# Kernel optimization log

Hardware: AMD Instinct MI355X
Metric: run time of the kernel (lower is better)

Reference implementation:

```python
import jax, jax.numpy as jnp
import numpy as np

N_NODES = 100000
N_USER = 50000
D_IN = 100     # n_units[0]
F_OUT = 16     # n_units[1]
N_HEAD = 3     # n_heads[0]
N_TYPES = 3    # nb_nodes
N_EDGES = 1600000
D2 = 128


def setup_inputs() -> dict:
    key = jax.random.key(0)
    ks = jax.random.split(key, 9)
    h = jax.random.normal(ks[0], (N_NODES, D_IN), dtype=jnp.float32)
    edge_index = jax.random.randint(ks[1], (N_TYPES, 2, N_EDGES), 0, N_NODES, dtype=jnp.int64)
    # per-type GAT params (torch Linear stored transposed: (in, out))
    W = jax.random.normal(ks[2], (N_TYPES, D_IN, N_HEAD * F_OUT), dtype=jnp.float32) * 0.1
    b = jax.random.normal(ks[3], (N_TYPES, N_HEAD * F_OUT), dtype=jnp.float32) * 0.1
    a_src = jax.random.normal(ks[4], (N_TYPES, N_HEAD, F_OUT), dtype=jnp.float32) * 0.1
    a_trg = jax.random.normal(ks[5], (N_TYPES, N_HEAD, F_OUT), dtype=jnp.float32) * 0.1
    # additive attention params
    w1 = jax.random.normal(ks[6], (D_IN, D2), dtype=jnp.float32) * 0.1
    w2 = jax.random.normal(ks[7], (F_OUT, D2), dtype=jnp.float32) * 0.1
    m = jax.random.normal(ks[8], (D2, 1), dtype=jnp.float32) * 0.1
    return {"h": h, "W": W, "b": b, "a_src": a_src, "a_trg": a_trg,
            "w1": w1, "w2": w2, "m": m, "edge_index": edge_index}


def _sparse_gat(h, src, trg, W, b, a_src, a_trg):
    """Single SparseMultiHeadGraphAttention layer followed by head-mean."""
    N = h.shape[0]
    h_prime = (h @ W + b).reshape(N, N_HEAD, F_OUT)  # (N, H, F)
    hs = h_prime[src]                                # (E', H, F) edge gather
    # NOTE: faithful to source — both scores use the src-gathered features
    e = (hs * a_src).sum(-1) + (hs * a_trg).sum(-1)  # (E', H)
    e = jax.nn.leaky_relu(e, negative_slope=0.2)
    e = e - e.max()                                  # global max (as in source)
    exp_e = jnp.exp(e)
    denom = jax.ops.segment_sum(exp_e, trg, num_segments=N)      # (N, H)
    alpha = exp_e / (denom[trg] + 1e-10)                          # (E', H)
    out = jax.ops.segment_sum(hs * alpha[..., None], trg, num_segments=N)  # (N, H, F)
    return out.mean(axis=1)  # == permute(1,0,2).mean(dim=0)


def reference(h, W, b, a_src, a_trg, w1, w2, m, edge_index):
    N = h.shape[0]
    loop = jnp.arange(N, dtype=edge_index.dtype)
    embs = []
    for t in range(N_TYPES):  # small fixed set of relation types
        src = jnp.concatenate([edge_index[t, 0], loop])  # add self-loops
        trg = jnp.concatenate([edge_index[t, 1], loop])
        x = _sparse_gat(h, src, trg, W[t], b[t], a_src[t], a_trg[t])
        embs.append(x[:N_USER])
    type_aware = jnp.stack(embs, axis=1)  # (Nu, |Rs|, F)
    feat = h[:N_USER]                     # (Nu, D)
    # additive attention over types
    q = jnp.tanh((feat @ w1)[:, None, :] + type_aware @ w2)  # (Nu, |Rs|, D2)
    scores = (q @ m)[..., 0]                                  # (Nu, |Rs|)
    beta = jax.nn.softmax(scores, axis=1)
    fusion = jnp.einsum('nr,nrf->nf', beta, type_aware)[:, None, :]  # (Nu,1,F)
    return jnp.concatenate([fusion, type_aware], axis=1)  # (Nu, |Rs|+1, F)
```

## Files before the change

kernel.cpp:

```cpp
#include <hip/hip_runtime.h>
#include <hip/hip_bf16.h>

#define N_NODES 100000
#define N_USER  50000
#define D_IN    100
#define F_OUT   16
#define N_HEAD  3
#define N_TYPES 3
#define N_EDGES 1600000
#define D2      128
#define N_SEG   (N_TYPES * N_USER)
#define KP      136
#define CAP     64
#define CAPH    32
#define NBLK    ((N_NODES + 63) / 64)
#define NPAIR   (N_TYPES * N_EDGES / 2)
#define NBIN    256
#define SEGB    586
#define NBLKA   782
#define PAIRS_A 3072
#define CAPPB   40
#define NPREPB  270
#define NPLACE  512

typedef __hip_bfloat16 bf16;
typedef __attribute__((ext_vector_type(8))) short bf16x8;
typedef __attribute__((ext_vector_type(4))) float f32x4;
static __device__ __forceinline__ float b2f(bf16 x) { return __bfloat162float(x); }
static __device__ __forceinline__ float us2f(ushort u) { return __uint_as_float(((unsigned)u) << 16); }

#define OFF_CVT   64
#define OFF_CW    (OFF_CVT)
#define OFF_CB    (OFF_CW + 14400)
#define OFF_CAS   (OFF_CB + 144)
#define OFF_CAT   (OFF_CAS + 144)
#define OFF_CW1   (OFF_CAT + 144)
#define OFF_CW2   (OFF_CW1 + 12800)
#define OFF_CM    (OFF_CW2 + 2048)
#define CVT_TOTAL 29808
#define OFF_WT    29888
#define OFF_REC   49472
#define OFF_BUCKET (OFF_REC + 9600000 + 240000 + 302000 + 9600000 + 2400000 + 6406144)
#define OFF_CPB   (OFF_REC + 9600000)
#define OFF_CA    (OFF_CPB + 240000)
#define OFF_CB2   (OFF_CA + 151000)
#define OFF_ELIST (OFF_CB2 + 151000)
#define OFF_TA    (OFF_ELIST + 9600000)
#define OFF_FW1   (OFF_TA + 2400000)

static __device__ __forceinline__ int2 load_ei2(const void* ei, int f64, size_t pairPos) {
    if (f64) {
        int4 v = ((const int4*)ei)[pairPos];
        int2 r; r.x = v.x; r.y = v.z; return r;
    }
    return ((const int2*)ei)[pairPos];
}

#define NBLK_CVT 117
__global__ __launch_bounds__(256) void k_prep_part(
        const void* __restrict__ W, const void* __restrict__ b,
        const void* __restrict__ as_, const void* __restrict__ at_,
        const void* __restrict__ w1, const void* __restrict__ w2,
        const void* __restrict__ m, const void* __restrict__ ei,
        const unsigned* __restrict__ hraw,
        float* __restrict__ cvt, ushort* __restrict__ wt,
        unsigned* __restrict__ bucket, unsigned* __restrict__ cpb) {
    __shared__ int bc[NBIN];
    __shared__ int s_sane, s_nz;
    const int tid = threadIdx.x;
    if (tid == 0) { s_sane = 0; s_nz = 0; }
    if (tid < NBIN) bc[tid] = 0;
    __syncthreads();
    {
        const unsigned* eir = (const unsigned*)ei;
        int cnt = 0; unsigned o = 0;
        for (int i = tid; i < 1024; i += 256) {
            unsigned w = hraw[i];
            unsigned e = (w >> 23) & 0xFF;
            if (e >= 64 && e <= 200) cnt++;
            o |= eir[2 * i + 1];
        }
        atomicAdd(&s_sane, cnt);
        atomicOr(&s_nz, (int)(o != 0));
    }
    __syncthreads();
    const int f32in = (s_sane > 512);
    const int f64ei = s_nz ? 0 : 1;
    if (blockIdx.x < NBLK_CVT) {
        int i = blockIdx.x * 256 + tid;
        if (i < CVT_TOTAL) {
            const void* src; int off;
            if      (i < 14400)                 { src = W;   off = i; }
            else if (i < 14400+144)             { src = b;   off = i - 14400; }
            else if (i < 14400+288)             { src = as_; off = i - 14544; }
            else if (i < 14400+432)             { src = at_; off = i - 14688; }
            else if (i < 14400+432+12800)       { src = w1;  off = i - 14832; }
            else if (i < 14400+432+12800+2048)  { src = w2;  off = i - 27632; }
            else                                { src = m;   off = i - 29680; }
            cvt[i] = f32in ? ((const float*)src)[off] : b2f(((const bf16*)src)[off]);
        }
    } else if (blockIdx.x < NPREPB) {
        int i = (blockIdx.x - NBLK_CVT) * 256 + tid;
        if (i < 6 * 48 * KP) {
            int g = i / (48 * KP);
            int r = i - g * (48 * KP);
            int n = r / KP, k = r % KP;
            ushort v = 0;
            if (k < D_IN) {
                if (g < 3) {
                    size_t src = ((size_t)g * D_IN + k) * 48 + n;
                    if (f32in) { bf16 x = __float2bfloat16(((const float*)W)[src]); v = *(ushort*)&x; }
                    else       { v = ((const ushort*)W)[src]; }
                } else {
                    int c = (g - 3) * 48 + n;
                    if (c < D2) {
                        size_t src = (size_t)k * D2 + c;
                        if (f32in) { bf16 x = __float2bfloat16(((const float*)w1)[src]); v = *(ushort*)&x; }
                        else       { v = ((const ushort*)w1)[src]; }
                    }
                }
            }
            wt[i] = v;
        }
    } else {
        const int blk = blockIdx.x - NPREPB;
        const int NE2 = N_EDGES >> 1;
        const int pair0 = blk * PAIRS_A;
        int npair = NPAIR - pair0; if (npair > PAIRS_A) npair = PAIRS_A;
#pragma unroll
        for (int q = 0; q < PAIRS_A / 256; ++q) {
            int pp = q * 256 + tid;
            int ok = (pp < npair);
            int pg = pair0 + (ok ? pp : 0);
            int t  = (pg >= 2 * NE2) ? 2 : ((pg >= NE2) ? 1 : 0);
            int ep = pg - t * NE2;
            int2 tg = load_ei2(ei, f64ei, (size_t)(t * 2 + 1) * NE2 + ep);
            int2 sr = load_ei2(ei, f64ei, (size_t)(t * 2) * NE2 + ep);
            if (ok && (unsigned)tg.x < N_USER) {
                int seg = t * N_USER + tg.x;
                int bin = seg & 255;
                int pos = atomicAdd(&bc[bin], 1);
                if (pos < CAPPB)
                    bucket[((size_t)bin * NBLKA + blk) * CAPPB + pos] =
                        ((unsigned)(seg >> 8) << 17) | (unsigned)sr.x;
            }
            if (ok && (unsigned)tg.y < N_USER) {
                int seg = t * N_USER + tg.y;
                int bin = seg & 255;
                int pos = atomicAdd(&bc[bin], 1);
                if (pos < CAPPB)
                    bucket[((size_t)bin * NBLKA + blk) * CAPPB + pos] =
                        ((unsigned)(seg >> 8) << 17) | (unsigned)sr.y;
            }
        }
        __syncthreads();
        if (tid < NBIN) cpb[(size_t)tid * NBLKA + blk] = (unsigned)bc[tid];
    }
}

__global__ __launch_bounds__(256) void k_place_pack(
        const unsigned* __restrict__ bucket, const unsigned* __restrict__ cpb,
        int* __restrict__ elist, unsigned* __restrict__ cA,
        unsigned* __restrict__ cBv,
        const void* __restrict__ h, const ushort* __restrict__ wtg,
        const float* __restrict__ cb, const float* __restrict__ cas,
        const float* __restrict__ cat,
        ushort* __restrict__ fw1G, float* __restrict__ rec) {
    __shared__ alignas(16) unsigned char smem[17408];
    __shared__ int s_sane;
    const int tid = threadIdx.x;
    if (blockIdx.x < NPLACE) {
        int* sc = (int*)smem;
        const int bin = blockIdx.x >> 1;
        const int hf  = blockIdx.x & 1;
        for (int i = tid; i < SEGB; i += 256) sc[i] = 0;
        __syncthreads();
        const int rn = NBLKA / 2;
        for (int j = tid; j < rn; j += 256) {
            int r = 2 * j + hf;
            int c = (int)cpb[(size_t)bin * NBLKA + r];
            if (c > CAPPB) c = CAPPB;
            size_t base = ((size_t)bin * NBLKA + r) * CAPPB;
            for (int i4 = 0; i4 < (c + 3) >> 2; ++i4) {
                uint4 wv = *(const uint4*)&bucket[base + 4 * i4];
#pragma unroll
                for (int k = 0; k < 4; ++k) {
                    int idx = 4 * i4 + k;
                    if (idx < c) {
                        unsigned e = (k == 0) ? wv.x : (k == 1) ? wv.y : (k == 2) ? wv.z : wv.w;
                        int sl  = (int)(e >> 17);
                        int src = (int)(e & 0x1FFFFu);
                        int pos = atomicAdd(&sc[sl], 1);
                        if (pos < CAPH) {
                            int seg = (sl << 8) + bin;
                            int t = seg / N_USER;
                            elist[(size_t)seg * CAP + (hf << 5) + pos] =
                                (t * N_NODES + src) << 7;
                        }
                    }
                }
            }
        }
        __syncthreads();
        for (int s = tid; s < SEGB; s += 256) {
            int seg = (s << 8) + bin;
            if (seg < N_SEG) {
                int cc = sc[s]; if (cc > CAPH) cc = CAPH;
                if (hf) cBv[seg] = (unsigned)cc; else cA[seg] = (unsigned)cc;
            }
        }
    } else {
        if (tid == 0) s_sane = 0;
        __syncthreads();
        {
            const unsigned* hraw = (const unsigned*)h;
            int cnt = 0;
            for (int i = tid; i < 1024; i += 256) {
                unsigned e = (hraw[i] >> 23) & 0xFF;
                if (e >= 64 && e <= 200) cnt++;
            }
            atomicAdd(&s_sane, cnt);
        }
        __syncthreads();
        const int f32in = (s_sane > 512);
        ushort (*hs)[KP] = reinterpret_cast<ushort(*)[KP]>(smem);
        const int node0 = (blockIdx.x - NPLACE) * 64;
        if (f32in) {
            const float* hfp = (const float*)h;
            for (int i = tid; i < 64 * 25; i += 256) {
                int r = i / 25, ch = i - r * 25;
                int n = node0 + r;
                ushort4 s4 = make_ushort4(0, 0, 0, 0);
                if (n < N_NODES) {
                    float4 x = *(const float4*)&hfp[(size_t)n * D_IN + ch * 4];
                    bf16 b0 = __float2bfloat16(x.x), b1 = __float2bfloat16(x.y);
                    bf16 b2 = __float2bfloat16(x.z), b3 = __float2bfloat16(x.w);
                    s4 = make_ushort4(*(ushort*)&b0, *(ushort*)&b1, *(ushort*)&b2, *(ushort*)&b3);
                }
                *(ushort4*)&hs[r][ch * 4] = s4;
            }
        } else {
            const ushort* hu = (const ushort*)h;
            for (int i = tid; i < 64 * 25; i += 256) {
                int r = i / 25, ch = i - r * 25;
                int n = node0 + r;
                uint2 v = make_uint2(0, 0);
                if (n < N_NODES)
                    v = *(const uint2*)&hu[(size_t)n * D_IN + ch * 4];
                *(uint2*)&hs[r][ch * 4] = v;
            }
        }
        for (int i = tid; i < 64 * 9; i += 256) {
            int r = i / 9, ch = i - r * 9;
            *(uint2*)&hs[r][100 + ch * 4] = make_uint2(0, 0);
        }
        __syncthreads();
        const int lane = tid & 63;
        const int w    = tid >> 6;
        const int m    = lane & 15;
        const int quad = lane >> 4;
        const int elig = (node0 < N_USER);
        const int nphase = elig ? 6 : 3;
        char* recc = (char*)rec;
        for (int p = 0; p < nphase; ++p) {
            const ushort* wp = wtg + (size_t)p * 48 * KP;
            f32x4 acc0 = {0.f, 0.f, 0.f, 0.f}, acc1 = acc0, acc2 = acc0;
#pragma unroll
            for (int ks = 0; ks < 4; ++ks) {
                int ko = ks * 32 + quad * 8;
                bf16x8 a  = *(const bf16x8*)&hs[w * 16 + m][ko];
                bf16x8 b0 = *(const bf16x8*)&wp[(0 * 16 + m) * KP + ko];
                bf16x8 b1 = *(const bf16x8*)&wp[(1 * 16 + m) * KP + ko];
                bf16x8 b2 = *(const bf16x8*)&wp[(2 * 16 + m) * KP + ko];
                acc0 = __builtin_amdgcn_mfma_f32_16x16x32_bf16(a, b0, acc0, 0, 0, 0);
                acc1 = __builtin_amdgcn_mfma_f32_16x16x32_bf16(a, b1, acc1, 0, 0, 0);
                acc2 = __builtin_amdgcn_mfma_f32_16x16x32_bf16(a, b2, acc2, 0, 0, 0);
            }
            if (p < 3) {
                const int t = p;
                float hpv[3][4], sred[3][4];
#pragma unroll
                for (int nt = 0; nt < 3; ++nt) {
                    int col = nt * 16 + m;
                    float bv = cb[t * 48 + col];
                    float av = cas[t * 48 + col] + cat[t * 48 + col];
                    f32x4 a4 = (nt == 0) ? acc0 : (nt == 1) ? acc1 : acc2;
#pragma unroll
                    for (int r = 0; r < 4; ++r) {
                        hpv[nt][r] = a4[r] + bv;
                        sred[nt][r] = hpv[nt][r] * av;
                    }
                }
#pragma unroll
                for (int d = 1; d < 16; d <<= 1) {
#pragma unroll
                    for (int nt = 0; nt < 3; ++nt)
#pragma unroll
                        for (int r = 0; r < 4; ++r)
                            sred[nt][r] += __shfl_xor(sred[nt][r], d);
                }
                float pk[3][4];
#pragma unroll
                for (int nt = 0; nt < 3; ++nt)
#pragma unroll
                    for (int r = 0; r < 4; ++r) {
                        float s = sred[nt][r];
                        s = (s > 0.f) ? s : 0.2f * s;
                        pk[nt][r] = __expf(s);
                    }
#pragma unroll
                for (int nt = 0; nt < 3; ++nt) {
                    int colb = (nt * 16 + m) * 2;
#pragma unroll
                    for (int r = 0; r < 4; ++r) {
                        int n = node0 + w * 16 + quad * 4 + r;
                        if (n < N_NODES) {
                            bf16 gb = __float2bfloat16(pk[nt][r] * hpv[nt][r]);
                            *(ushort*)(recc + (((size_t)t * N_NODES + n) << 7) + colb) = *(ushort*)&gb;
                        }
                    }
                }
                if (m < 3) {
#pragma unroll
                    for (int r = 0; r < 4; ++r) {
                        int n = node0 + w * 16 + quad * 4 + r;
                        if (n < N_NODES)
                            *(float*)(recc + (((size_t)t * N_NODES + n) << 7) + 96 + m * 4) = pk[m][r];
                    }
                }
            } else {
                const int chunk = p - 3;
#pragma unroll
                for (int nt = 0; nt < 3; ++nt) {
                    int col = chunk * 48 + nt * 16 + m;
                    if (col < D2) {
                        f32x4 a4 = (nt == 0) ? acc0 : (nt == 1) ? acc1 : acc2;
#pragma unroll
                        for (int r = 0; r < 4; ++r) {
                            int row = w * 16 + quad * 4 + r;
                            int v = node0 + row;
                            if (v < N_USER) {
                                bf16 fb = __float2bfloat16(a4[r]);
                                fw1G[(size_t)v * D2 + col] = *(ushort*)&fb;
                            }
                        }
                    }
                }
            }
        }
    }
}

__global__ __launch_bounds__(256) void k_gather(const float* __restrict__ rec,
                                                const int* __restrict__ elist,
                                                const unsigned* __restrict__ cA,
                                                const unsigned* __restrict__ cBv,
                                                float* __restrict__ ta) {
    int wid = (blockIdx.x * 256 + threadIdx.x) >> 6;
    if (wid >= N_SEG) return;
    int lane = threadIdx.x & 63;
    int t = wid / N_USER, v = wid - t * N_USER;
    int h = lane >> 5, l = lane & 31;
    const char* recc = (const char*)rec;
    const unsigned l4 = (unsigned)(l << 2);
    const bool isg = (l < 24);
    const int      s0m = isg ? 16 : 0;
    const unsigned m0  = isg ? 0xFFFF0000u : 0xFFFFFFFFu;
    const unsigned m1  = isg ? 0xFFFF0000u : 0u;
    int ev = elist[(size_t)wid * CAP + lane];
    int a = (int)cA[wid];
    int b = (int)cBv[wid];
    unsigned wself = 0u;
    if (h == 0)
        wself = *(const unsigned*)(recc + (((unsigned)(t * N_NODES + v)) << 7) + l4);
    float a0 = 0.f, a1 = 0.f;
    const int myn = h ? b : a;
    const int mx = a > b ? a : b;
    const int hbase = h << 5;
    for (int i0 = 0; i0 < mx; i0 += 12) {
        unsigned w[12];
#pragma unroll
        for (int q = 0; q < 12; ++q) {
            w[q] = 0u;
            int ee = i0 + q;
            int off = __shfl(ev, hbase + (ee & 31));
            if (ee < myn)
                w[q] = *(const unsigned*)(recc + (unsigned)off + l4);
        }
        __builtin_amdgcn_sched_barrier(0);
#pragma unroll
        for (int q = 0; q < 12; ++q) {
            a0 += __uint_as_float((w[q] << s0m) & m0);
            a1 += __uint_as_float(w[q] & m1);
        }
    }
    a0 += __uint_as_float((wself << s0m) & m0);
    a1 += __uint_as_float(wself & m1);
    a0 += __shfl_xor(a0, 32);
    a1 += __shfl_xor(a1, 32);
    int k = (l >> 3); if (k > 2) k = 2;
    float dk = __shfl(a0, 24 + k) + 1e-10f;
    float r0 = a0 / dk, r1 = a1 / dk;
    float sf0 = r0 + __shfl(r0, (l & 7) + 8) + __shfl(r0, (l & 7) + 16);
    float sf1 = r1 + __shfl(r1, (l & 7) + 8) + __shfl(r1, (l & 7) + 16);
    if (lane < 8) {
        float2 o;
        o.x = sf0 * (1.f / 3.f);
        o.y = sf1 * (1.f / 3.f);
        *(float2*)&ta[(size_t)v * 48 + t * 16 + 2 * lane] = o;
    }
}

__global__ __launch_bounds__(256) void k_fuse(const ushort* __restrict__ fw1G,
                                              const float* __restrict__ cw2,
                                              const float* __restrict__ cm,
                                              const float* __restrict__ ta,
                                              const unsigned* __restrict__ hraw,
                                              void* __restrict__ out) {
    __shared__ float w2s[F_OUT * D2];
    __shared__ float ms[D2];
    __shared__ float tas[64][49];
    __shared__ float psum[64][12];
    __shared__ float fus[64][16];
    __shared__ int s_sane;
    const int tid = threadIdx.x;
    const int v0 = blockIdx.x * 64;
    if (tid == 0) s_sane = 0;
    __syncthreads();
    {
        int cnt = 0;
        for (int i = tid; i < 1024; i += 256) {
            unsigned e = (hraw[i] >> 23) & 0xFF;
            if (e >= 64 && e <= 200) cnt++;
        }
        atomicAdd(&s_sane, cnt);
    }
    for (int i = tid; i < F_OUT * D2; i += 256) w2s[i] = cw2[i];
    if (tid < D2) ms[tid] = cm[tid];
    {
        int r = tid >> 2, c4 = (tid & 3) * 12;
        int v = v0 + r;
        for (int j = 0; j < 12; ++j)
            tas[r][c4 + j] = (v < N_USER) ? ta[(size_t)v * 48 + c4 + j] : 0.f;
    }
    __syncthreads();
    const int f32in = (s_sane > 512);
    const int u  = tid & 63;
    const int og = tid >> 6;
    const int v  = v0 + u;
    float tr[48];
#pragma unroll
    for (int x = 0; x < 48; ++x) tr[x] = tas[u][x];
    float acc[2][16];
#pragma unroll
    for (int ph = 0; ph < 2; ++ph) {
        if (v < N_USER) {
            const ushort* fr = fw1G + (size_t)v * D2 + ph * 64 + og * 16;
            ushort us[16];
            *(uint4*)&us[0] = *(const uint4*)&fr[0];
            *(uint4*)&us[8] = *(const uint4*)&fr[8];
#pragma unroll
            for (int j = 0; j < 16; ++j) acc[ph][j] = us2f(us[j]);
        } else {
#pragma unroll
            for (int j = 0; j < 16; ++j) acc[ph][j] = 0.f;
        }
    }
    float part[3] = {0.f, 0.f, 0.f};
#pragma unroll
    for (int ph = 0; ph < 2; ++ph) {
#pragma unroll
        for (int j = 0; j < 16; ++j) {
            int c = ph * 64 + og * 16 + j;
            float fv = acc[ph][j];
            float mv = ms[c];
#pragma unroll
            for (int t = 0; t < 3; ++t) {
                float z = fv;
#pragma unroll
                for (int f = 0; f < 16; ++f)
                    z += tr[t * 16 + f] * w2s[f * D2 + c];
                float q = 1.f - 2.f / (__expf(2.f * z) + 1.f);
                part[t] += q * mv;
            }
        }
    }
    psum[u][og * 3 + 0] = part[0];
    psum[u][og * 3 + 1] = part[1];
    psum[u][og * 3 + 2] = part[2];
    __syncthreads();
    if (tid < 64) {
        float sc[3];
#pragma unroll
        for (int t = 0; t < 3; ++t)
            sc[t] = psum[tid][t] + psum[tid][3 + t] + psum[tid][6 + t] + psum[tid][9 + t];
        float mx = fmaxf(sc[0], fmaxf(sc[1], sc[2]));
        float e0 = __expf(sc[0] - mx), e1 = __expf(sc[1] - mx), e2 = __expf(sc[2] - mx);
        float inv = 1.f / (e0 + e1 + e2);
#pragma unroll
        for (int f = 0; f < 16; ++f)
            fus[tid][f] = (e0 * tas[tid][f] + e1 * tas[tid][16 + f] + e2 * tas[tid][32 + f]) * inv;
    }
    __syncthreads();
    for (int kq = 0; kq < 16; ++kq) {
        int lin = kq * 256 + tid;
        int r = lin >> 6, c = lin & 63;
        int vv = v0 + r;
        if (vv < N_USER) {
            float val = (c < 16) ? fus[r][c] : tas[r][c - 16];
            size_t oidx = (size_t)vv * 64 + c;
            if (f32in) ((float*)out)[oidx] = val;
            else       ((bf16*)out)[oidx]  = __float2bfloat16(val);
        }
    }
}

extern "C" void kernel_launch(void* const* d_in, const int* in_sizes, int n_in,
                              void* d_out, int out_size, void* d_ws, size_t ws_size,
                              hipStream_t stream) {
    float* ws = (float*)d_ws;
    float* cvt   = ws + OFF_CVT;
    float* cb    = ws + OFF_CB;
    float* cas   = ws + OFF_CAS;
    float* cat   = ws + OFF_CAT;
    float* cw2   = ws + OFF_CW2;
    float* cm    = ws + OFF_CM;
    ushort* wt   = (ushort*)(ws + OFF_WT);
    float* rec   = ws + OFF_REC;
    unsigned* bucket = (unsigned*)(ws + OFF_BUCKET);
    unsigned* cpb    = (unsigned*)(ws + OFF_CPB);
    unsigned* cA     = (unsigned*)(ws + OFF_CA);
    unsigned* cBv    = (unsigned*)(ws + OFF_CB2);
    int*   elist = (int*)(ws + OFF_ELIST);
    float* ta    = ws + OFF_TA;
    ushort* fw1  = (ushort*)(ws + OFF_FW1);

    k_prep_part<<<NPREPB + NBLKA, 256, 0, stream>>>(
        d_in[1], d_in[2], d_in[3], d_in[4], d_in[5], d_in[6], d_in[7], d_in[8],
        (const unsigned*)d_in[0], cvt, wt, bucket, cpb);

    k_place_pack<<<NPLACE + NBLK, 256, 0, stream>>>(
        bucket, cpb, elist, cA, cBv,
        d_in[0], wt, cb, cas, cat, fw1, rec);

    k_gather<<<(N_SEG * 64 + 255) / 256, 256, 0, stream>>>(rec, elist, cA, cBv, ta);

    k_fuse<<<(N_USER + 63) / 64, 256, 0, stream>>>(
        fw1, cw2, cm, ta, (const unsigned*)d_in[0], d_out);
}
```

Before: 358.4 us.

## Fuse four pipeline kernels into one cooperative persistent kernel with grid syncs

Merges the prep/partition, place/pack, gather and fuse kernels into a single cooperative kernel that grid-strides over each stage's blocks and separates stages with grid-wide syncs. This removes three kernel launches and the idle gaps between them. The grid is sized from the occupancy query, capped at 8 blocks per CU times 256 CUs, and falls back to the old multi-kernel path if the cooperative launch fails. The risk is that grid syncs and persistent looping cut parallelism or occupancy in the gather-heavy stages, since every block also reserves about 21 KB of shared memory.

After: 375.8 us. 1.05x slower.

```diff
diff --git a/kernel.cpp b/kernel.cpp
--- a/kernel.cpp
+++ b/kernel.cpp
@@ -1,5 +1,8 @@
 #include <hip/hip_runtime.h>
 #include <hip/hip_bf16.h>
+#include <hip/hip_cooperative_groups.h>
+
+namespace cg = cooperative_groups;
 
 #define N_NODES 100000
 #define N_USER  50000
@@ -22,6 +25,8 @@
 #define CAPPB   40
 #define NPREPB  270
 #define NPLACE  512
+#define NFUSE   ((N_USER + 63) / 64)
+#define NBLK_CVT 117
 
 typedef __hip_bfloat16 bf16;
 typedef __attribute__((ext_vector_type(8))) short bf16x8;
@@ -30,8 +35,7 @@
 static __device__ __forceinline__ float us2f(ushort u) { return __uint_as_float(((unsigned)u) << 16); }
 
 #define OFF_CVT   64
-#define OFF_CW    (OFF_CVT)
-#define OFF_CB    (OFF_CW + 14400)
+#define OFF_CB    (OFF_CVT + 14400)
 #define OFF_CAS   (OFF_CB + 144)
 #define OFF_CAT   (OFF_CAS + 144)
 #define OFF_CW1   (OFF_CAT + 144)
@@ -56,7 +60,435 @@
     return ((const int2*)ei)[pairPos];
 }
 
-#define NBLK_CVT 117
+struct MegaArgs {
+    const void *h, *W, *b, *as_, *at_, *w1, *w2, *m, *ei;
+    float* cvt; ushort* wt;
+    unsigned *bucket, *cpb, *cA, *cBv;
+    int* elist;
+    float* ta; ushort* fw1; float* rec;
+    const float *cb, *cas, *cat, *cw2, *cm;
+    void* out;
+};
+
+__global__ __launch_bounds__(256) void kmega(MegaArgs A) {
+    __shared__ alignas(16) unsigned char arena[21248];
+    __shared__ int s_flags[2];
+    const int tid = threadIdx.x;
+    const int bid = blockIdx.x;
+    const int gs  = gridDim.x;
+    cg::grid_group gg = cg::this_grid();
+    if (tid == 0) { s_flags[0] = 0; s_flags[1] = 0; }
+    __syncthreads();
+    {
+        const unsigned* hraw = (const unsigned*)A.h;
+        const unsigned* eir  = (const unsigned*)A.ei;
+        int cnt = 0; unsigned o = 0;
+        for (int i = tid; i < 1024; i += 256) {
+            unsigned e = (hraw[i] >> 23) & 0xFF;
+            cnt += (e >= 64 && e <= 200) ? 1 : 0;
+            o |= eir[2 * i + 1];
+        }
+        atomicAdd(&s_flags[0], cnt);
+        atomicOr(&s_flags[1], (int)(o != 0));
+    }
+    __syncthreads();
+    const int f32in = (s_flags[0] > 512);
+    const int f64ei = s_flags[1] ? 0 : 1;
+    for (int u = bid; u < NPREPB + NBLKA; u += gs) {
+        if (u < NBLK_CVT) {
+            int i = u * 256 + tid;
+            if (i < CVT_TOTAL) {
+                const void* src; int off;
+                if      (i < 14400)                 { src = A.W;   off = i; }
+                else if (i < 14400+144)             { src = A.b;   off = i - 14400; }
+                else if (i < 14400+288)             { src = A.as_; off = i - 14544; }
+                else if (i < 14400+432)             { src = A.at_; off = i - 14688; }
+                else if (i < 14400+432+12800)       { src = A.w1;  off = i - 14832; }
+                else if (i < 14400+432+12800+2048)  { src = A.w2;  off = i - 27632; }
+                else                                { src = A.m;   off = i - 29680; }
+                A.cvt[i] = f32in ? ((const float*)src)[off] : b2f(((const bf16*)src)[off]);
+            }
+        } else if (u < NPREPB) {
+            int i = (u - NBLK_CVT) * 256 + tid;
+            if (i < 6 * 48 * KP) {
+                int g = i / (48 * KP);
+                int r = i - g * (48 * KP);
+                int n = r / KP, k = r % KP;
+                ushort v = 0;
+                if (k < D_IN) {
+                    if (g < 3) {
+                        size_t src = ((size_t)g * D_IN + k) * 48 + n;
+                        if (f32in) { bf16 x = __float2bfloat16(((const float*)A.W)[src]); v = *(ushort*)&x; }
+                        else       { v = ((const ushort*)A.W)[src]; }
+                    } else {
+                        int c = (g - 3) * 48 + n;
+                        if (c < D2) {
+                            size_t src = (size_t)k * D2 + c;
+                            if (f32in) { bf16 x = __float2bfloat16(((const float*)A.w1)[src]); v = *(ushort*)&x; }
+                            else       { v = ((const ushort*)A.w1)[src]; }
+                        }
+                    }
+                }
+                A.wt[i] = v;
+            }
+        } else {
+            const int blk = u - NPREPB;
+            int* bc = (int*)arena;
+            __syncthreads();
+            for (int i = tid; i < NBIN; i += 256) bc[i] = 0;
+            __syncthreads();
+            const int NE2 = N_EDGES >> 1;
+            const int pair0 = blk * PAIRS_A;
+            int npair = NPAIR - pair0; if (npair > PAIRS_A) npair = PAIRS_A;
+#pragma unroll
+            for (int q = 0; q < PAIRS_A / 256; ++q) {
+                int pp = q * 256 + tid;
+                int ok = (pp < npair);
+                int pg = pair0 + (ok ? pp : 0);
+                int t  = (pg >= 2 * NE2) ? 2 : ((pg >= NE2) ? 1 : 0);
+                int ep = pg - t * NE2;
+                int2 tg = load_ei2(A.ei, f64ei, (size_t)(t * 2 + 1) * NE2 + ep);
+                int2 sr = load_ei2(A.ei, f64ei, (size_t)(t * 2) * NE2 + ep);
+                if (ok && (unsigned)tg.x < N_USER) {
+                    int seg = t * N_USER + tg.x;
+                    int bin = seg & 255;
+                    int pos = atomicAdd(&bc[bin], 1);
+                    if (pos < CAPPB)
+                        A.bucket[((size_t)bin * NBLKA + blk) * CAPPB + pos] =
+                            ((unsigned)(seg >> 8) << 17) | (unsigned)sr.x;
+                }
+                if (ok && (unsigned)tg.y < N_USER) {
+                    int seg = t * N_USER + tg.y;
+                    int bin = seg & 255;
+                    int pos = atomicAdd(&bc[bin], 1);
+                    if (pos < CAPPB)
+                        A.bucket[((size_t)bin * NBLKA + blk) * CAPPB + pos] =
+                            ((unsigned)(seg >> 8) << 17) | (unsigned)sr.y;
+                }
+            }
+            __syncthreads();
+            if (tid < NBIN) A.cpb[(size_t)tid * NBLKA + blk] = (unsigned)bc[tid];
+        }
+    }
+    __threadfence();
+    gg.sync();
+    for (int u = bid; u < NPLACE + NBLK; u += gs) {
+        if (u < NPLACE) {
+            int* sc = (int*)arena;
+            const int bin = u >> 1;
+            const int hf  = u & 1;
+            __syncthreads();
+            for (int i = tid; i < SEGB; i += 256) sc[i] = 0;
+            __syncthreads();
+            const int rn = NBLKA / 2;
+            for (int j = tid; j < rn; j += 256) {
+                int r = 2 * j + hf;
+                int c = (int)A.cpb[(size_t)bin * NBLKA + r];
+                if (c > CAPPB) c = CAPPB;
+                size_t base = ((size_t)bin * NBLKA + r) * CAPPB;
+                for (int i4 = 0; i4 < (c + 3) >> 2; ++i4) {
+                    uint4 wv = *(const uint4*)&A.bucket[base + 4 * i4];
+#pragma unroll
+                    for (int k = 0; k < 4; ++k) {
+                        int idx = 4 * i4 + k;
+                        if (idx < c) {
+                            unsigned e = (k == 0) ? wv.x : (k == 1) ? wv.y : (k == 2) ? wv.z : wv.w;
+                            int sl  = (int)(e >> 17);
+                            int src = (int)(e & 0x1FFFFu);
+                            int pos = atomicAdd(&sc[sl], 1);
+                            if (pos < CAPH) {
+                                int seg = (sl << 8) + bin;
+                                int t = seg / N_USER;
+                                A.elist[(size_t)seg * CAP + (hf << 5) + pos] =
+                                    (t * N_NODES + src) << 7;
+                            }
+                        }
+                    }
+                }
+            }
+            __syncthreads();
+            for (int s = tid; s < SEGB; s += 256) {
+                int seg = (s << 8) + bin;
+                if (seg < N_SEG) {
+                    int cc = sc[s]; if (cc > CAPH) cc = CAPH;
+                    if (hf) A.cBv[seg] = (unsigned)cc; else A.cA[seg] = (unsigned)cc;
+                }
+            }
+        } else {
+            ushort (*hs)[KP] = reinterpret_cast<ushort(*)[KP]>(arena);
+            const int node0 = (u - NPLACE) * 64;
+            __syncthreads();
+            if (f32in) {
+                const float* hfp = (const float*)A.h;
+                for (int i = tid; i < 64 * 25; i += 256) {
+                    int r = i / 25, ch = i - r * 25;
+                    int n = node0 + r;
+                    ushort4 s4 = make_ushort4(0, 0, 0, 0);
+                    if (n < N_NODES) {
+                        float4 x = *(const float4*)&hfp[(size_t)n * D_IN + ch * 4];
+                        bf16 b0 = __float2bfloat16(x.x), b1 = __float2bfloat16(x.y);
+                        bf16 b2 = __float2bfloat16(x.z), b3 = __float2bfloat16(x.w);
+                        s4 = make_ushort4(*(ushort*)&b0, *(ushort*)&b1, *(ushort*)&b2, *(ushort*)&b3);
+                    }
+                    *(ushort4*)&hs[r][ch * 4] = s4;
+                }
+            } else {
+                const ushort* hu = (const ushort*)A.h;
+                for (int i = tid; i < 64 * 25; i += 256) {
+                    int r = i / 25, ch = i - r * 25;
+                    int n = node0 + r;
+                    uint2 v = make_uint2(0, 0);
+                    if (n < N_NODES)
+                        v = *(const uint2*)&hu[(size_t)n * D_IN + ch * 4];
+                    *(uint2*)&hs[r][ch * 4] = v;
+                }
+            }
+            for (int i = tid; i < 64 * 9; i += 256) {
+                int r = i / 9, ch = i - r * 9;
+                *(uint2*)&hs[r][100 + ch * 4] = make_uint2(0, 0);
+            }
+            __syncthreads();
+            const int lane = tid & 63;
+            const int w    = tid >> 6;
+            const int m    = lane & 15;
+            const int quad = lane >> 4;
+            const int elig = (node0 < N_USER);
+            const int nphase = elig ? 6 : 3;
+            char* recc = (char*)A.rec;
+            for (int p = 0; p < nphase; ++p) {
+                const ushort* wp = A.wt + (size_t)p * 48 * KP;
+                f32x4 acc0 = {0.f, 0.f, 0.f, 0.f}, acc1 = acc0, acc2 = acc0;
+#pragma unroll
+                for (int ks = 0; ks < 4; ++ks) {
+                    int ko = ks * 32 + quad * 8;
+                    bf16x8 a  = *(const bf16x8*)&hs[w * 16 + m][ko];
+                    bf16x8 b0 = *(const bf16x8*)&wp[(0 * 16 + m) * KP + ko];
+                    bf16x8 b1 = *(const bf16x8*)&wp[(1 * 16 + m) * KP + ko];
+                    bf16x8 b2 = *(const bf16x8*)&wp[(2 * 16 + m) * KP + ko];
+                    acc0 = __builtin_amdgcn_mfma_f32_16x16x32_bf16(a, b0, acc0, 0, 0, 0);
+                    acc1 = __builtin_amdgcn_mfma_f32_16x16x32_bf16(a, b1, acc1, 0, 0, 0);
+                    acc2 = __builtin_amdgcn_mfma_f32_16x16x32_bf16(a, b2, acc2, 0, 0, 0);
+                }
+                if (p < 3) {
+                    const int t = p;
+                    float hpv[3][4], sred[3][4];
+#pragma unroll
+                    for (int nt = 0; nt < 3; ++nt) {
+                        int col = nt * 16 + m;
+                        float bv = A.cb[t * 48 + col];
+                        float av = A.cas[t * 48 + col] + A.cat[t * 48 + col];
+                        f32x4 a4 = (nt == 0) ? acc0 : (nt == 1) ? acc1 : acc2;
+#pragma unroll
+                        for (int r = 0; r < 4; ++r) {
+                            hpv[nt][r] = a4[r] + bv;
+                            sred[nt][r] = hpv[nt][r] * av;
+                        }
+                    }
+#pragma unroll
+                    for (int d = 1; d < 16; d <<= 1) {
+#pragma unroll
+                        for (int nt = 0; nt < 3; ++nt)
+#pragma unroll
+                            for (int r = 0; r < 4; ++r)
+                                sred[nt][r] += __shfl_xor(sred[nt][r], d);
+                    }
+                    float pk[3][4];
+#pragma unroll
+                    for (int nt = 0; nt < 3; ++nt)
+#pragma unroll
+                        for (int r = 0; r < 4; ++r) {
+                            float s = sred[nt][r];
+                            s = (s > 0.f) ? s : 0.2f * s;
+                            pk[nt][r] = __expf(s);
+                        }
+#pragma unroll
+                    for (int nt = 0; nt < 3; ++nt) {
+                        int colb = (nt * 16 + m) * 2;
+#pragma unroll
+                        for (int r = 0; r < 4; ++r) {
+                            int n = node0 + w * 16 + quad * 4 + r;
+                            if (n < N_NODES) {
+                                bf16 gb = __float2bfloat16(pk[nt][r] * hpv[nt][r]);
+                                *(ushort*)(recc + (((size_t)t * N_NODES + n) << 7) + colb) = *(ushort*)&gb;
+                            }
+                        }
+                    }
+                    if (m < 3) {
+#pragma unroll
+                        for (int r = 0; r < 4; ++r) {
+                            int n = node0 + w * 16 + quad * 4 + r;
+                            if (n < N_NODES)
+                                *(float*)(recc + (((size_t)t * N_NODES + n) << 7) + 96 + m * 4) = pk[m][r];
+                        }
+                    }
+                } else {
+                    const int chunk = p - 3;
+#pragma unroll
+                    for (int nt = 0; nt < 3; ++nt) {
+                        int col = chunk * 48 + nt * 16 + m;
+                        if (col < D2) {
+                            f32x4 a4 = (nt == 0) ? acc0 : (nt == 1) ? acc1 : acc2;
+#pragma unroll
+                            for (int r = 0; r < 4; ++r) {
+                                int row = w * 16 + quad * 4 + r;
+                                int v = node0 + row;
+                                if (v < N_USER) {
+                                    bf16 fb = __float2bfloat16(a4[r]);
+                                    A.fw1[(size_t)v * D2 + col] = *(ushort*)&fb;
+                                }
+                            }
+                        }
+                    }
+                }
+            }
+        }
+    }
+    __threadfence();
+    gg.sync();
+    {
+        const int wv   = tid >> 6;
+        const int lane = tid & 63;
+        const int h = lane >> 5, l = lane & 31;
+        const char* recc = (const char*)A.rec;
+        const unsigned l4 = (unsigned)(l << 2);
+        const bool isg = (l < 24);
+        const int      s0m = isg ? 16 : 0;
+        const unsigned m0  = isg ? 0xFFFF0000u : 0xFFFFFFFFu;
+        const unsigned m1  = isg ? 0xFFFF0000u : 0u;
+        for (int wid = bid * 4 + wv; wid < N_SEG; wid += gs * 4) {
+            int t = wid / N_USER, v = wid - t * N_USER;
+            int ev = A.elist[(size_t)wid * CAP + lane];
+            int a = (int)A.cA[wid];
+            int b = (int)A.cBv[wid];
+            unsigned wself = 0u;
+            if (h == 0)
+                wself = *(const unsigned*)(recc + (((unsigned)(t * N_NODES + v)) << 7) + l4);
+            float a0 = 0.f, a1 = 0.f;
+            const int myn = h ? b : a;
+            const int mx = a > b ? a : b;
+            const int hbase = h << 5;
+            for (int i0 = 0; i0 < mx; i0 += 12) {
+                unsigned w[12];
+#pragma unroll
+                for (int q = 0; q < 12; ++q) {
+                    w[q] = 0u;
+                    int ee = i0 + q;
+                    int off = __shfl(ev, hbase + (ee & 31));
+                    if (ee < myn)
+                        w[q] = *(const unsigned*)(recc + (unsigned)off + l4);
+                }
+                __builtin_amdgcn_sched_barrier(0);
+#pragma unroll
+                for (int q = 0; q < 12; ++q) {
+                    a0 += __uint_as_float((w[q] << s0m) & m0);
+                    a1 += __uint_as_float(w[q] & m1);
+                }
+            }
+            a0 += __uint_as_float((wself << s0m) & m0);
+            a1 += __uint_as_float(wself & m1);
+            a0 += __shfl_xor(a0, 32);
+            a1 += __shfl_xor(a1, 32);
+            int k = (l >> 3); if (k > 2) k = 2;
+            float dk = __shfl(a0, 24 + k) + 1e-10f;
+            float r0 = a0 / dk, r1 = a1 / dk;
+            float sf0 = r0 + __shfl(r0, (l & 7) + 8) + __shfl(r0, (l & 7) + 16);
+            float sf1 = r1 + __shfl(r1, (l & 7) + 8) + __shfl(r1, (l & 7) + 16);
+            if (lane < 8) {
+                float2 o;
+                o.x = sf0 * (1.f / 3.f);
+                o.y = sf1 * (1.f / 3.f);
+                *(float2*)&A.ta[(size_t)v * 48 + t * 16 + 2 * lane] = o;
+            }
+        }
+    }
+    __threadfence();
+    gg.sync();
+    for (int u = bid; u < NFUSE; u += gs) {
+        float* w2s = (float*)arena;
+        float* ms  = (float*)(arena + 8192);
+        float (*tas)[49] = (float(*)[49])(arena + 8704);
+        float (*psum)[12] = (float(*)[12])arena;
+        float (*fus)[16]  = (float(*)[16])(arena + 3072);
+        const int v0 = u * 64;
+        __syncthreads();
+        for (int i = tid; i < F_OUT * D2; i += 256) w2s[i] = A.cw2[i];
+        if (tid < D2) ms[tid] = A.cm[tid];
+        {
+            int r = tid >> 2, c4 = (tid & 3) * 12;
+            int v = v0 + r;
+            for (int j = 0; j < 12; ++j)
+                tas[r][c4 + j] = (v < N_USER) ? A.ta[(size_t)v * 48 + c4 + j] : 0.f;
+        }
+        __syncthreads();
+        const int uu = tid & 63;
+        const int og = tid >> 6;
+        const int v  = v0 + uu;
+        float tr[48];
+#pragma unroll
+        for (int x = 0; x < 48; ++x) tr[x] = tas[uu][x];
+        float part[3] = {0.f, 0.f, 0.f};
+#pragma unroll
+        for (int ph = 0; ph < 2; ++ph) {
+            float acc[16];
+            if (v < N_USER) {
+                const ushort* fr = A.fw1 + (size_t)v * D2 + ph * 64 + og * 16;
+                ushort us[16];
+                *(uint4*)&us[0] = *(const uint4*)&fr[0];
+                *(uint4*)&us[8] = *(const uint4*)&fr[8];
+#pragma unroll
+                for (int j = 0; j < 16; ++j) acc[j] = us2f(us[j]);
+            } else {
+#pragma unroll
+                for (int j = 0; j < 16; ++j) acc[j] = 0.f;
+            }
+#pragma unroll
+            for (int j = 0; j < 16; ++j) {
+                int c = ph * 64 + og * 16 + j;
+                float fv = acc[j];
+                float mv = ms[c];
+#pragma unroll
+                for (int t = 0; t < 3; ++t) {
+                    float z = fv;
+#pragma unroll
+                    for (int f = 0; f < 16; ++f)
+                        z += tr[t * 16 + f] * w2s[f * D2 + c];
+                    float q = 1.f - 2.f / (__expf(2.f * z) + 1.f);
+                    part[t] += q * mv;
+                }
+            }
+        }
+        __syncthreads();
+        psum[uu][og * 3 + 0] = part[0];
+        psum[uu][og * 3 + 1] = part[1];
+        psum[uu][og * 3 + 2] = part[2];
+        __syncthreads();
+        if (tid < 64) {
+            float sc3[3];
+#pragma unroll
+            for (int t = 0; t < 3; ++t)
+                sc3[t] = psum[tid][t] + psum[tid][3 + t] + psum[tid][6 + t] + psum[tid][9 + t];
+            float mx = fmaxf(sc3[0], fmaxf(sc3[1], sc3[2]));
+            float e0 = __expf(sc3[0] - mx), e1 = __expf(sc3[1] - mx), e2 = __expf(sc3[2] - mx);
+            float inv = 1.f / (e0 + e1 + e2);
+#pragma unroll
+            for (int f = 0; f < 16; ++f)
+                fus[tid][f] = (e0 * tas[tid][f] + e1 * tas[tid][16 + f] + e2 * tas[tid][32 + f]) * inv;
+        }
+        __syncthreads();
+        for (int kq = 0; kq < 16; ++kq) {
+            int lin = kq * 256 + tid;
+            int r = lin >> 6, c = lin & 63;
+            int vv = v0 + r;
+            if (vv < N_USER) {
+                float val = (c < 16) ? fus[r][c] : tas[r][c - 16];
+                size_t oidx = (size_t)vv * 64 + c;
+                if (f32in) ((float*)A.out)[oidx] = val;
+                else       ((bf16*)A.out)[oidx]  = __float2bfloat16(val);
+            }
+        }
+    }
+}
+
 __global__ __launch_bounds__(256) void k_prep_part(
         const void* __restrict__ W, const void* __restrict__ b,
         const void* __restrict__ as_, const void* __restrict__ at_,
@@ -451,28 +883,25 @@
     float tr[48];
 #pragma unroll
     for (int x = 0; x < 48; ++x) tr[x] = tas[u][x];
-    float acc[2][16];
+    float part[3] = {0.f, 0.f, 0.f};
 #pragma unroll
     for (int ph = 0; ph < 2; ++ph) {
+        float acc[16];
         if (v < N_USER) {
             const ushort* fr = fw1G + (size_t)v * D2 + ph * 64 + og * 16;
             ushort us[16];
             *(uint4*)&us[0] = *(const uint4*)&fr[0];
             *(uint4*)&us[8] = *(const uint4*)&fr[8];
 #pragma unroll
-            for (int j = 0; j < 16; ++j) acc[ph][j] = us2f(us[j]);
+            for (int j = 0; j < 16; ++j) acc[j] = us2f(us[j]);
         } else {
 #pragma unroll
-            for (int j = 0; j < 16; ++j) acc[ph][j] = 0.f;
-        }
-    }
-    float part[3] = {0.f, 0.f, 0.f};
-#pragma unroll
-    for (int ph = 0; ph < 2; ++ph) {
+            for (int j = 0; j < 16; ++j) acc[j] = 0.f;
+        }
 #pragma unroll
         for (int j = 0; j < 16; ++j) {
             int c = ph * 64 + og * 16 + j;
-            float fv = acc[ph][j];
+            float fv = acc[j];
             float mv = ms[c];
 #pragma unroll
             for (int t = 0; t < 3; ++t) {
@@ -535,6 +964,32 @@
     float* ta    = ws + OFF_TA;
     ushort* fw1  = (ushort*)(ws + OFF_FW1);
 
+    static int g_coop = -1;
+    if (g_coop != 0) {
+        static int g_maxb = 0;
+        if (g_maxb == 0) {
+            int mb = 0;
+            if (hipOccupancyMaxActiveBlocksPerMultiprocessor(&mb, kmega, 256, 0) == hipSuccess && mb > 0)
+                g_maxb = (mb > 8) ? 8 : mb;
+            else
+                g_maxb = 4;
+        }
+        MegaArgs margs;
+        margs.h = d_in[0]; margs.W = d_in[1]; margs.b = d_in[2];
+        margs.as_ = d_in[3]; margs.at_ = d_in[4]; margs.w1 = d_in[5];
+        margs.w2 = d_in[6]; margs.m = d_in[7]; margs.ei = d_in[8];
+        margs.cvt = cvt; margs.wt = wt; margs.bucket = bucket; margs.cpb = cpb;
+        margs.cA = cA; margs.cBv = cBv; margs.elist = elist;
+        margs.ta = ta; margs.fw1 = fw1; margs.rec = rec;
+        margs.cb = cb; margs.cas = cas; margs.cat = cat; margs.cw2 = cw2; margs.cm = cm;
+        margs.out = d_out;
+        void* params[1] = { (void*)&margs };
+        hipError_t err = hipLaunchCooperativeKernel(kmega, dim3(g_maxb * 256), dim3(256),
+                                                    params, 0, stream);
+        if (err == hipSuccess) { g_coop = 1; return; }
+        g_coop = 0;
+    }
+
     k_prep_part<<<NPREPB + NBLKA, 256, 0, stream>>>(
         d_in[1], d_in[2], d_in[3], d_in[4], d_in[5], d_in[6], d_in[7], d_in[8],
         (const unsigned*)d_in[0], cvt, wt, bucket, cpb);
```
